# Kernel tuning notes

Hardware: AMD Instinct MI355X
Metric: run time of the kernel (lower is better)

## Reference

```python
import jax, jax.numpy as jnp
import numpy as np

B, N, F, H, E = 32, 512, 256, 1024, 8192
LN_EPS = 1e-5


def setup_inputs() -> dict:
    key = jax.random.key(0)
    ks = jax.random.split(key, 8)
    s = 0.02
    return {
        "node_features": jax.random.normal(ks[0], (B, N, F), jnp.float32),
        "edge_indexd": jax.random.randint(ks[1], (2, E), 0, N, jnp.int64),
        "edge_weights": jax.random.uniform(ks[2], (B, E), jnp.float32),
        "ln_gamma": jnp.ones((F,), jnp.float32),
        "ln_beta": jnp.zeros((F,), jnp.float32),
        "w1": jax.random.normal(ks[3], (H, N), jnp.float32) * s,
        "b1": jnp.zeros((H,), jnp.float32),
        "w2": jax.random.normal(ks[4], (N, H), jnp.float32) * s,
        "b2": jnp.zeros((N,), jnp.float32),
    }


def _laplacian(edge_idx, w):
    # w: [E] edge weights for one graph; edge_idx: [2, E]
    w = jnp.clip(w, 0.0, 1.0)
    # sparse_coo_tensor(...).to_dense() sums duplicate indices -> scatter-add
    A = jnp.zeros((N, N), w.dtype).at[edge_idx[0], edge_idx[1]].add(w)
    A = (A + A.T) * 0.5
    deg = jnp.clip(A.sum(axis=1), 1e-6, None)
    dis = deg ** -0.5  # finite since deg >= 1e-6
    L = jnp.eye(N, dtype=w.dtype) - dis[:, None] * A * dis[None, :]
    L = (L + L.T) * 0.5 + 1e-6 * jnp.eye(N, dtype=w.dtype)
    return L


def _forward(node_features, edge_indexd, edge_weights, ln_gamma, ln_beta, w1, b1, w2, b2):
    L = jax.vmap(lambda w: _laplacian(edge_indexd, w))(edge_weights)  # [B,N,N]
    # eigh is applied to L.detach() in the original -> stop_gradient
    eigvals, eigvecs = jnp.linalg.eigh(jax.lax.stop_gradient(L))  # [B,N], [B,N,N]

    # LayerNorm over feat_dim
    mu = node_features.mean(-1, keepdims=True)
    var = node_features.var(-1, keepdims=True)
    x = (node_features - mu) * jax.lax.rsqrt(var + LN_EPS) * ln_gamma + ln_beta
    x_residual = x
    x = jax.nn.relu(x)

    # x1 = eigvecs^T @ x : [B,N,F]
    x1 = jnp.einsum('bnk,bnf->bkf', eigvecs, x)
    # MLP on eigenvalues (dropout inactive in eval)
    h = jax.nn.relu(eigvals @ w1.T + b1)  # [B,H]
    ev_feat = h @ w2.T + b2               # [B,N]
    x1 = x1 * ev_feat[:, :, None]
    out = jnp.einsum('bnk,bkf->bnf', eigvecs, x1) + x_residual
    return out


def reference(node_features, edge_indexd, edge_weights, ln_gamma, ln_beta, w1, b1, w2, b2):
    return _forward(node_features, edge_indexd, edge_weights, ln_gamma, ln_beta, w1, b1, w2, b2)
```

## Files before the change

kernel.cpp:

```cpp
#include <hip/hip_runtime.h>
#include <math.h>

#define BDIM 32
#define NDIM 512
#define FDIM 256
#define HDIM 1024
#define EDIM 8192
#define PCH  8192
#define CLTH 1.2e-4f
#define NB   16
#define BCOLS 16

__device__ __forceinline__ float waveRedSum(float v){
#pragma unroll
  for(int o=32;o>0;o>>=1) v += __shfl_down(v,o,64);
  return v;
}

__device__ __forceinline__ float rnd_f(int g, int i){
  unsigned s = (unsigned)g*1315423911u ^ (unsigned)i*2654435761u;
  s ^= s>>13; s *= 2246822519u; s ^= s>>16;
  return (float)(s & 0xFFFF)*(1.f/65536.f) - 0.5f;
}

__global__ __launch_bounds__(1024) void k_detect(const unsigned* __restrict__ e, int* __restrict__ flag){
  int t = threadIdx.x;
  float c = 0.f;
  for(int i=t;i<EDIM;i+=1024) if(e[2*i+1] != 0u) c += 1.f;
  c = waveRedSum(c);
  __shared__ float r[16];
  if((t&63)==0) r[t>>6]=c;
  __syncthreads();
  if(t==0){ float s=0; for(int z=0;z<16;z++) s+=r[z]; flag[0] = (s>64.f)?1:0; }
}

__global__ __launch_bounds__(256) void k_scatter(const float* __restrict__ ew, const int* __restrict__ eidx,
                                                 const int* __restrict__ flag, float* __restrict__ A){
  int t = blockIdx.x*256 + threadIdx.x;
  int b = t>>13, e = t&(EDIM-1);
  int i, j;
  if(flag[0]){ i = eidx[e]; j = eidx[EDIM+e]; }
  else       { i = eidx[2*e]; j = eidx[2*(EDIM+e)]; }
  i &= 511; j &= 511;
  float w = ew[(size_t)b*EDIM + e];
  w = 0.5f*fminf(fmaxf(w,0.f),1.f);
  float* Ab = A + (size_t)b*NDIM*NDIM;
  atomicAdd(Ab + (size_t)i*NDIM + j, w);
  atomicAdd(Ab + (size_t)j*NDIM + i, w);
}

__global__ __launch_bounds__(256) void k_degree(const float* __restrict__ A, float* __restrict__ dis){
  int wid = threadIdx.x>>6, lane = threadIdx.x&63;
  int row = blockIdx.x*4 + wid;
  const float* Ar = A + (size_t)row*NDIM;
  float s = 0.f;
  for(int j=lane;j<NDIM;j+=64) s += Ar[j];
  s = waveRedSum(s);
  if(lane==0) dis[row] = rsqrtf(fmaxf(s, 1e-6f));
}

__global__ __launch_bounds__(256) void k_lap(float* __restrict__ A, const float* __restrict__ dis){
  size_t t = (size_t)blockIdx.x*256 + threadIdx.x;
  size_t nn = (size_t)NDIM*NDIM;
  int b = (int)(t / nn); size_t rem = t % nn;
  int i = (int)(rem / NDIM), j = (int)(rem % NDIM);
  float v = -dis[b*NDIM+i]*dis[b*NDIM+j]*A[t];
  if(i==j) v += 1.f + 1e-6f;
  A[t] = v;
}

__global__ __launch_bounds__(256) void k_ln(const float* __restrict__ nf, const float* __restrict__ g,
                                            const float* __restrict__ be, float* __restrict__ X){
  int wid = threadIdx.x>>6, lane = threadIdx.x&63;
  int row = blockIdx.x*4 + wid;
  const float4* r4 = (const float4*)(nf + (size_t)row*FDIM);
  float4 v = r4[lane];
  float s  = v.x+v.y+v.z+v.w;
  float s2 = v.x*v.x+v.y*v.y+v.z*v.z+v.w*v.w;
  s = waveRedSum(s); s2 = waveRedSum(s2);
  s = __shfl(s,0,64); s2 = __shfl(s2,0,64);
  float mean = s*(1.f/FDIM);
  float var  = s2*(1.f/FDIM) - mean*mean;
  float inv  = rsqrtf(var + 1e-5f);
  float4 gg = ((const float4*)g)[lane];
  float4 bb = ((const float4*)be)[lane];
  float4 o;
  o.x = (v.x-mean)*inv*gg.x + bb.x;
  o.y = (v.y-mean)*inv*gg.y + bb.y;
  o.z = (v.z-mean)*inv*gg.z + bb.z;
  o.w = (v.w-mean)*inv*gg.w + bb.w;
  ((float4*)(X + (size_t)row*FDIM))[lane] = o;
}

__global__ __launch_bounds__(512,1) void k_tridiag(float* __restrict__ A, float* __restrict__ U,
                                                   float* __restrict__ dia, float* __restrict__ off,
                                                   float* __restrict__ tau){
  const int b = blockIdx.x, t = threadIdx.x;
  float* Ab = A + (size_t)b*NDIM*NDIM;
  float* Ub = U + (size_t)b*NDIM*NDIM;
  __shared__ __align__(16) float Up[NB][NDIM];
  __shared__ __align__(16) float Wp[NB][NDIM];
  __shared__ __align__(16) float ps[4][NDIM];
  __shared__ float dW[NB], dU[NB];
  __shared__ float sig_s, pd_s, x0_s;
  const int lane = t&63;
  const int cc = t&127, rg = t>>7;
  if(t==0){ sig_s = 0.f; pd_s = 0.f; }

  for(int k0=0; k0<NDIM-2; k0+=NB){
    const int ne = (NB < NDIM-2-k0)? NB : (NDIM-2-k0);
    for(int q=0;q<NB;q++){ Up[q][t]=0.f; Wp[q][t]=0.f; }
    __syncthreads();
    for(int p=0;p<ne;p++){
      const int k = k0+p;
      float v = 0.f;
      if(t>k){
        v = Ab[(size_t)k*NDIM + t];
        for(int q=0;q<p;q++) v -= Up[q][k]*Wp[q][t] + Wp[q][k]*Up[q][t];
      }
      if(t<NB){ dW[t]=0.f; dU[t]=0.f; }
      if(t==0) pd_s = 0.f;
      if(t==k+1) x0_s = v;
      float ssq = (t>=k+2)? v*v : 0.f;
      ssq = waveRedSum(ssq);
      if(lane==0) atomicAdd(&sig_s, ssq);
      __syncthreads();
      const float sigma = sig_s, x0 = x0_s;
      float tk = 0.f, inv = 0.f, beta = x0;
      if(sigma > 1e-26f){
        beta = -copysignf(sqrtf(x0*x0+sigma), x0);
        tk = (beta-x0)/beta; inv = 1.f/(x0-beta);
      }
      const float u_t = (t>=k+2)? v*inv : ((t==k+1 && sigma>1e-26f)? 1.f : 0.f);
      Up[p][t] = u_t;
      for(int q=0;q<p;q++){
        float pw = waveRedSum(Wp[q][t]*u_t);
        float pu = waveRedSum(Up[q][t]*u_t);
        if(lane==0){ atomicAdd(&dW[q],pw); atomicAdd(&dU[q],pu); }
      }
      __syncthreads();
      if(t==0) sig_s = 0.f;
      {
        float4 acc = {0.f,0.f,0.f,0.f};
        const int j0 = 4*cc;
        if(j0+3 > k){
          const float* basep = Ab + j0;
          const int ib0 = (k+1)&~31;
          const int i1 = rg*4, i2 = 16+rg*4;
          const float* ap = basep + (size_t)ib0*NDIM;
          float4 c0 = *(const float4*)(ap + (size_t)(i1  )*NDIM);
          float4 c1 = *(const float4*)(ap + (size_t)(i1+1)*NDIM);
          float4 c2 = *(const float4*)(ap + (size_t)(i1+2)*NDIM);
          float4 c3 = *(const float4*)(ap + (size_t)(i1+3)*NDIM);
          float4 d0 = *(const float4*)(ap + (size_t)(i2  )*NDIM);
          float4 d1 = *(const float4*)(ap + (size_t)(i2+1)*NDIM);
          float4 d2 = *(const float4*)(ap + (size_t)(i2+2)*NDIM);
          float4 d3 = *(const float4*)(ap + (size_t)(i2+3)*NDIM);
          for(int ib=ib0; ib<NDIM; ib+=32){
            float4 n0=c0,n1=c1,n2=c2,n3=c3,m0=d0,m1=d1,m2=d2,m3=d3;
            if(ib+32 < NDIM){
              const float* an = basep + (size_t)(ib+32)*NDIM;
              n0 = *(const float4*)(an + (size_t)(i1  )*NDIM);
              n1 = *(const float4*)(an + (size_t)(i1+1)*NDIM);
              n2 = *(const float4*)(an + (size_t)(i1+2)*NDIM);
              n3 = *(const float4*)(an + (size_t)(i1+3)*NDIM);
              m0 = *(const float4*)(an + (size_t)(i2  )*NDIM);
              m1 = *(const float4*)(an + (size_t)(i2+1)*NDIM);
              m2 = *(const float4*)(an + (size_t)(i2+2)*NDIM);
              m3 = *(const float4*)(an + (size_t)(i2+3)*NDIM);
            }
            float4 u1 = *(const float4*)&Up[p][ib+i1];
            float4 u2 = *(const float4*)&Up[p][ib+i2];
            acc.x += c0.x*u1.x + c1.x*u1.y + c2.x*u1.z + c3.x*u1.w
                   + d0.x*u2.x + d1.x*u2.y + d2.x*u2.z + d3.x*u2.w;
            acc.y += c0.y*u1.x + c1.y*u1.y + c2.y*u1.z + c3.y*u1.w
                   + d0.y*u2.x + d1.y*u2.y + d2.y*u2.z + d3.y*u2.w;
            acc.z += c0.z*u1.x + c1.z*u1.y + c2.z*u1.z + c3.z*u1.w
                   + d0.z*u2.x + d1.z*u2.y + d2.z*u2.z + d3.z*u2.w;
            acc.w += c0.w*u1.x + c1.w*u1.y + c2.w*u1.z + c3.w*u1.w
                   + d0.w*u2.x + d1.w*u2.y + d2.w*u2.z + d3.w*u2.w;
            c0=n0; c1=n1; c2=n2; c3=n3; d0=m0; d1=m1; d2=m2; d3=m3;
          }
        }
        *(float4*)&ps[rg][4*cc] = acc;
      }
      __syncthreads();
      float py = ps[0][t]+ps[1][t]+ps[2][t]+ps[3][t];
      float corr = 0.f;
      for(int q=0;q<p;q++) corr += Up[q][t]*dW[q] + Wp[q][t]*dU[q];
      float pv = tk*(py - corr);
      float pdp = waveRedSum(pv*u_t);
      if(lane==0) atomicAdd(&pd_s, pdp);
      __syncthreads();
      float hh = 0.5f*tk*pd_s;
      float w_t = (t>k)? (pv - hh*u_t) : 0.f;
      Wp[p][t] = w_t;
      if(t>k) Ub[(size_t)k*NDIM + (t-k-1)] = u_t;
      if(t==0){
        off[(size_t)b*NDIM+k] = beta; tau[(size_t)b*NDIM+k] = tk;
        float dk = Ab[(size_t)k*NDIM+k];
        for(int q=0;q<p;q++) dk -= 2.f*Up[q][k]*Wp[q][k];
        dia[(size_t)b*NDIM+k]=dk;
      }
      __syncthreads();
    }
    {
      const int r0 = k0+ne;
      const int rbase = r0 & ~15;
      const int cstart = rbase>>2;
      if(cc >= cstart){
        const int j0 = 4*cc;
        for(int rt=rbase; rt<NDIM; rt+=16){
          const int i0 = rt + rg*4;
          float* a0 = Ab + (size_t)i0*NDIM + j0;
          float4 v0 = *(float4*)(a0);
          float4 v1 = *(float4*)(a0+NDIM);
          float4 v2 = *(float4*)(a0+2*NDIM);
          float4 v3 = *(float4*)(a0+3*NDIM);
          #pragma unroll 4
          for(int q=0;q<ne;q++){
            float4 Ui = *(const float4*)&Up[q][i0];
            float4 Wi = *(const float4*)&Wp[q][i0];
            float4 Uj = *(const float4*)&Up[q][j0];
            float4 Wj = *(const float4*)&Wp[q][j0];
            v0.x -= Ui.x*Wj.x + Wi.x*Uj.x; v0.y -= Ui.x*Wj.y + Wi.x*Uj.y; v0.z -= Ui.x*Wj.z + Wi.x*Uj.z; v0.w -= Ui.x*Wj.w + Wi.x*Uj.w;
            v1.x -= Ui.y*Wj.x + Wi.y*Uj.x; v1.y -= Ui.y*Wj.y + Wi.y*Uj.y; v1.z -= Ui.y*Wj.z + Wi.y*Uj.z; v1.w -= Ui.y*Wj.w + Wi.y*Uj.w;
            v2.x -= Ui.z*Wj.x + Wi.z*Uj.x; v2.y -= Ui.z*Wj.y + Wi.z*Uj.y; v2.z -= Ui.z*Wj.z + Wi.z*Uj.z; v2.w -= Ui.z*Wj.w + Wi.z*Uj.w;
            v3.x -= Ui.w*Wj.x + Wi.w*Uj.x; v3.y -= Ui.w*Wj.y + Wi.w*Uj.y; v3.z -= Ui.w*Wj.z + Wi.w*Uj.z; v3.w -= Ui.w*Wj.w + Wi.w*Uj.w;
          }
          *(float4*)(a0)        = v0;
          *(float4*)(a0+NDIM)   = v1;
          *(float4*)(a0+2*NDIM) = v2;
          *(float4*)(a0+3*NDIM) = v3;
        }
      }
    }
    __syncthreads();
  }
  if(t==0){
    dia[(size_t)b*NDIM+NDIM-2] = Ab[(size_t)(NDIM-2)*NDIM+NDIM-2];
    dia[(size_t)b*NDIM+NDIM-1] = Ab[(size_t)(NDIM-1)*NDIM+NDIM-1];
    off[(size_t)b*NDIM+NDIM-2] = Ab[(size_t)(NDIM-2)*NDIM+NDIM-1];
    off[(size_t)b*NDIM+NDIM-1] = 0.f;
    tau[(size_t)b*NDIM+NDIM-2]=0.f; tau[(size_t)b*NDIM+NDIM-1]=0.f;
  }
}

__global__ __launch_bounds__(512) void k_bisect(const float* __restrict__ dia, const float* __restrict__ off,
                                                float* __restrict__ lam){
  int b = blockIdx.x, t = threadIdx.x;
  __shared__ float ds[NDIM], e2[NDIM];
  __shared__ float red[16];
  __shared__ float slo, shi;
  ds[t] = dia[(size_t)b*NDIM+t];
  float ev = (t<NDIM-1)? off[(size_t)b*NDIM+t] : 0.f;
  e2[t] = ev*ev;
  __syncthreads();
  float el = (t>0)? sqrtf(e2[t-1]) : 0.f;
  float er = fabsf(ev);
  float lo = ds[t]-el-er, hi = ds[t]+el+er;
#pragma unroll
  for(int o=32;o>0;o>>=1){ lo = fminf(lo,__shfl_down(lo,o,64)); hi = fmaxf(hi,__shfl_down(hi,o,64)); }
  if((t&63)==0){ red[t>>6]=lo; red[8+(t>>6)]=hi; }
  __syncthreads();
  if(t==0){
    float L=red[0], H=red[8];
    for(int z=1;z<8;z++){ L=fminf(L,red[z]); H=fmaxf(H,red[8+z]); }
    slo = L-1e-3f; shi = H+1e-3f;
  }
  __syncthreads();
  float lo2 = slo, hi2 = shi;
  for(int it=0; it<30; ++it){
    float mid = 0.5f*(lo2+hi2);
    float q = ds[0]-mid; int c = (q<0.f)?1:0;
    for(int i=1;i<NDIM;i++){
      float dn = (fabsf(q)<1e-10f)? ((q<0.f)?-1e-10f:1e-10f) : q;
      q = ds[i]-mid - __fdividef(e2[i-1], dn);
      c += (q<0.f)?1:0;
    }
    if(c<=t) lo2=mid; else hi2=mid;
  }
  lam[(size_t)b*NDIM+t] = 0.5f*(lo2+hi2);
}

__global__ __launch_bounds__(64) void k_stein(const float* __restrict__ dia, const float* __restrict__ off,
                                              const float* __restrict__ lam, float* __restrict__ W,
                                              float* __restrict__ fac, float* __restrict__ xs, int chunk){
  int p = blockIdx.x*64 + threadIdx.x;
  int g = chunk*PCH + p;
  int b = g >> 9, j = g & 511;
  __shared__ float ds[NDIM], es[NDIM];
  for(int i=threadIdx.x;i<NDIM;i+=64){ ds[i]=dia[(size_t)b*NDIM+i]; es[i]=off[(size_t)b*NDIM+i]; }
  __syncthreads();
  float lm = lam[(size_t)b*NDIM+j] + (float)((j%5)-2)*1.2e-7f;
  float* fu = fac + p;
  float* fm = fac + (size_t)PCH*NDIM + p;
  float* f1a = xs + p;
  float ai = ds[0]-lm, bi = es[0];
  for(int ib=0; ib<NDIM-1; ib+=8){
    const int lim = (NDIM-1-ib < 8)? NDIM-1-ib : 8;
    float dsb[8], esb[8], enb[8];
    #pragma unroll
    for(int z=0;z<8;z++){
      int i = ib+z; bool vz = z<lim;
      dsb[z] = vz? ds[i+1] : 0.f;
      esb[z] = vz? es[i]   : 0.f;
      enb[z] = (vz && i<NDIM-2)? es[i+1] : 0.f;
    }
    #pragma unroll
    for(int z=0;z<8;z++){
      if(z<lim){
        int i = ib+z;
        float ci = esb[z], an = dsb[z]-lm, bn = enb[z];
        float uu, mmenc, s1;
        if(fabsf(ai) >= fabsf(ci)){
          float aa = (fabsf(ai)<1e-12f)? ((ai<0.f)?-1e-12f:1e-12f) : ai;
          float mm = __fdividef(ci, aa);
          uu=aa; mmenc=mm; s1=bi;
          ai = an - mm*bi; bi = bn;
        } else {
          float cch = (fabsf(ci)<1e-12f)? ((ci<0.f)?-1e-12f:1e-12f) : ci;
          float mm = __fdividef(ai, cch);
          uu=cch; mmenc=mm+3.f; s1=an;
          ai = bi - mm*an; bi = -mm*bn;
        }
        fu[(size_t)i*PCH]=__fdividef(1.f,uu);
        fm[(size_t)i*PCH]=mmenc;
        f1a[(size_t)i*PCH]=s1;
      }
    }
  }
  { float aa = (fabsf(ai)<1e-12f)? ((ai<0.f)?-1e-12f:1e-12f) : ai; fu[(size_t)(NDIM-1)*PCH]=__fdividef(1.f,aa); }
  float* Wb = W + (size_t)b*NDIM*NDIM + j;
  float scale = 1.f;
  for(int it=0; it<3; ++it){
    float yi = (it==0)? rnd_f(g,0) : Wb[0]*scale;
    for(int ib=0; ib<NDIM-1; ib+=8){
      const int lim = (NDIM-1-ib < 8)? NDIM-1-ib : 8;
      float wn[8], me[8];
      #pragma unroll
      for(int z=0;z<8;z++){
        int i = ib+z; bool vz = z<lim;
        wn[z] = vz? ((it==0)? rnd_f(g,i+1) : Wb[(size_t)(i+1)*NDIM]*scale) : 0.f;
        me[z] = vz? fm[(size_t)i*PCH] : 0.f;
      }
      #pragma unroll
      for(int z=0;z<8;z++){
        if(z<lim){
          int i = ib+z;
          float enc = me[z]; bool sw = enc>1.5f; float mm = sw? enc-3.f : enc;
          float yn = wn[z];
          if(sw){ float tmp=yi; yi=yn; yn=tmp; }
          yn -= mm*yi;
          Wb[(size_t)i*NDIM] = yi;
          yi = yn;
        }
      }
    }
    float nrm, xp1, xp2;
    {
      float xi = yi * fu[(size_t)(NDIM-1)*PCH];
      Wb[(size_t)(NDIM-1)*NDIM]=xi; nrm = xi*xi; xp2=0.f; xp1=xi;
    }
    for(int ib=NDIM-2; ib>=0; ib-=8){
      const int lim = (ib+1 < 8)? ib+1 : 8;
      float yv[8], ru[8], me[8], f1b[8];
      #pragma unroll
      for(int z=0;z<8;z++){
        int i = ib-z; bool vz = z<lim;
        yv[z]  = vz? Wb[(size_t)i*NDIM] : 0.f;
        ru[z]  = vz? fu[(size_t)i*PCH] : 0.f;
        me[z]  = vz? fm[(size_t)i*PCH] : 0.f;
        f1b[z] = vz? f1a[(size_t)i*PCH] : 0.f;
      }
      #pragma unroll
      for(int z=0;z<8;z++){
        if(z<lim){
          int i = ib-z;
          bool sw = me[z]>1.5f;
          float f2 = sw? ((i<NDIM-2)? es[i+1] : 0.f) : 0.f;
          float xi = (yv[z] - f1b[z]*xp1 - f2*xp2)*ru[z];
          Wb[(size_t)i*NDIM]=xi; nrm += xi*xi;
          xp2=xp1; xp1=xi;
        }
      }
    }
    scale = rsqrtf(fmaxf(nrm,1e-30f));
  }
  for(int ib=0; ib<NDIM; ib+=8){
    float vz[8];
    #pragma unroll
    for(int z=0;z<8;z++) vz[z] = Wb[(size_t)(ib+z)*NDIM];
    #pragma unroll
    for(int z=0;z<8;z++) Wb[(size_t)(ib+z)*NDIM] = vz[z]*scale;
  }
}

__global__ __launch_bounds__(512) void k_mgs(const float* __restrict__ lam, float* __restrict__ W){
  int b = blockIdx.x, t = threadIdx.x;
  __shared__ int cstart[NDIM];
  __shared__ unsigned char brk[NDIM];
  __shared__ float red[8];
  __shared__ float sbc;
  const float* lb = lam + (size_t)b*NDIM;
  float* Wb = W + (size_t)b*NDIM*NDIM;
  brk[t] = (t==0)? 1 : ((lb[t]-lb[t-1] > CLTH)? 1 : 0);
  __syncthreads();
  if(t==0){ int s=0; for(int j=0;j<NDIM;j++){ if(brk[j]) s=j; cstart[j]=s; } }
  __syncthreads();
  for(int j=1;j<NDIM;j++){
    int s = cstart[j];
    if(s==j) continue;
    for(int q=s;q<j;q++){
      float pd = 0.f;
      pd = Wb[(size_t)t*NDIM+q]*Wb[(size_t)t*NDIM+j];
      pd = waveRedSum(pd);
      if((t&63)==0) red[t>>6]=pd;
      __syncthreads();
      if(t==0){ float s2=0; for(int z=0;z<8;z++) s2+=red[z]; sbc=s2; }
      __syncthreads();
      float dt = sbc;
      Wb[(size_t)t*NDIM+j] -= dt*Wb[(size_t)t*NDIM+q];
      __syncthreads();
    }
    float v = Wb[(size_t)t*NDIM+j];
    float pn = waveRedSum(v*v);
    if((t&63)==0) red[t>>6]=pn;
    __syncthreads();
    if(t==0){ float s2=0; for(int z=0;z<8;z++) s2+=red[z]; sbc=s2; }
    __syncthreads();
    Wb[(size_t)t*NDIM+j] = v*rsqrtf(fmaxf(sbc,1e-20f));
    __syncthreads();
  }
}

__global__ __launch_bounds__(512,4) void k_backt(float* __restrict__ W, const float* __restrict__ U,
                                                 const float* __restrict__ tau){
  __shared__ float S[NDIM][BCOLS+1];
  __shared__ float Up[NB][516];
  __shared__ float Gp[NB][NB+1];
  __shared__ float Tm[NB][NB+1];
  __shared__ float Yp[2][NB][NB+1];
  __shared__ float Z16[NB][NB+1];
  __shared__ float tls[NB];
  const int t = threadIdx.x;
  int b = blockIdx.x >> 5, slab = blockIdx.x & 31;
  int c0 = slab*BCOLS;
  float* Wb = W + (size_t)b*NDIM*NDIM;
  const float* Ub = U + (size_t)b*NDIM*NDIM;
  for(int l=t; l<NDIM*BCOLS; l+=512){
    int i = l>>4, c = l&15;
    S[i][c] = Wb[(size_t)i*NDIM + c0 + c];
  }
  __syncthreads();
  for(int k0 = ((NDIM-3)/NB)*NB; k0>=0; k0-=NB){
    for(int l=t; l<NB*NDIM; l+=512){
      int q = l>>9, i = l&511;
      int k = k0+q;
      float v = 0.f;
      if(k < NDIM-2 && i > k) v = Ub[(size_t)k*NDIM + (i-k-1)];
      Up[q][i] = v;
    }
    if(t<NB) tls[t] = (k0+t < NDIM-2)? tau[(size_t)b*NDIM + k0 + t] : 0.f;
    if(t<NB*(NB+1)) ((float*)Gp)[t] = 0.f;
    __syncthreads();
    if(t < 480){
      int pp = t>>2, sub = t&3;
      int pj=1, pr=pp;
      while(pr >= pj){ pr -= pj; pj++; }
      int s = pr, jj = pj;
      float acc = 0.f;
      for(int i=k0+1+sub; i<NDIM; i+=4) acc += Up[s][i]*Up[jj][i];
      atomicAdd(&Gp[s][jj], acc);
    }
    __syncthreads();
    if(t < 16){
      int a = t;
      for(int j=0;j<NB;j++){
        float v;
        if(a==j) v = tls[j];
        else if(a<j){
          float s2 = 0.f;
          for(int s=a; s<j; s++) s2 += Tm[a][s]*Gp[s][j];
          v = -tls[j]*s2;
        } else v = 0.f;
        Tm[a][j] = v;
      }
    }
    __syncthreads();
    {
      int q=(t>>4)&15, c=t&15, half=t>>8;
      float a0=0.f, a1=0.f;
      int i = k0+1+half;
      for(; i+2<NDIM; i+=4){ a0 += Up[q][i]*S[i][c]; a1 += Up[q][i+2]*S[i+2][c]; }
      for(; i<NDIM; i+=2) a0 += Up[q][i]*S[i][c];
      Yp[half][q][c] = a0+a1;
    }
    __syncthreads();
    if(t < 256){
      int a=t>>4, c=t&15;
      float acc=0.f;
      #pragma unroll
      for(int j=0;j<NB;j++) acc += Tm[a][j]*(Yp[0][j][c]+Yp[1][j][c]);
      Z16[a][c]=acc;
    }
    __syncthreads();
    {
      int rg=t>>4, c=t&15;
      float zc[NB];
      #pragma unroll
      for(int q=0;q<NB;q++) zc[q]=Z16[q][c];
      for(int i=k0+1+rg; i<NDIM; i+=32){
        float s2=0.f;
        #pragma unroll
        for(int q=0;q<NB;q++) s2 += Up[q][i]*zc[q];
        S[i][c] -= s2;
      }
    }
    __syncthreads();
  }
  for(int l=t; l<NDIM*BCOLS; l+=512){
    int i = l>>4, c = l&15;
    Wb[(size_t)i*NDIM + c0 + c] = S[i][c];
  }
}

__global__ __launch_bounds__(256) void k_mlp1(const float* __restrict__ lam, const float* __restrict__ w1,
                                              const float* __restrict__ b1, float* __restrict__ h){
  int wid = threadIdx.x>>6, lane = threadIdx.x&63;
  int j = blockIdx.x*4 + wid, b = blockIdx.y;
  const float* lb = lam + (size_t)b*NDIM;
  const float* wr = w1 + (size_t)j*NDIM;
  float acc = 0.f;
  for(int k=lane;k<NDIM;k+=64) acc += lb[k]*wr[k];
  acc = waveRedSum(acc);
  if(lane==0) h[(size_t)b*HDIM + j] = fmaxf(acc + b1[j], 0.f);
}
__global__ __launch_bounds__(256) void k_mlp2(const float* __restrict__ h, const float* __restrict__ w2,
                                              const float* __restrict__ b2, float* __restrict__ evb){
  int wid = threadIdx.x>>6, lane = threadIdx.x&63;
  int n = blockIdx.x*4 + wid, b = blockIdx.y;
  const float* hb = h + (size_t)b*HDIM;
  const float* wr = w2 + (size_t)n*HDIM;
  float acc = 0.f;
  for(int k=lane;k<HDIM;k+=64) acc += hb[k]*wr[k];
  acc = waveRedSum(acc);
  if(lane==0) evb[(size_t)b*NDIM + n] = acc + b2[n];
}

__global__ __launch_bounds__(256) void k_gemm1(const float* __restrict__ Z, const float* __restrict__ X,
                                               const float* __restrict__ evb, float* __restrict__ X1){
  int b = blockIdx.z;
  int i0 = blockIdx.y*64, f0 = blockIdx.x*64;
  const float* Zb = Z + (size_t)b*NDIM*NDIM;
  const float* Xb = X + (size_t)b*NDIM*FDIM;
  __shared__ float As[32][65], Bs[32][65];
  int tx = threadIdx.x & 15, ty = threadIdx.x >> 4;
  float acc[4][4] = {};
  for(int n0=0;n0<NDIM;n0+=32){
    for(int l=threadIdx.x; l<32*64; l+=256){
      int dn = l>>6, dc = l&63;
      As[dn][dc] = Zb[(size_t)(n0+dn)*NDIM + i0+dc];
      Bs[dn][dc] = fmaxf(Xb[(size_t)(n0+dn)*FDIM + f0+dc], 0.f);
    }
    __syncthreads();
#pragma unroll
    for(int dn=0;dn<32;dn++){
      float a[4], bb[4];
#pragma unroll
      for(int z=0;z<4;z++){ a[z]=As[dn][ty*4+z]; bb[z]=Bs[dn][tx*4+z]; }
#pragma unroll
      for(int p=0;p<4;p++)
#pragma unroll
        for(int q=0;q<4;q++) acc[p][q] += a[p]*bb[q];
    }
    __syncthreads();
  }
#pragma unroll
  for(int p=0;p<4;p++){
    int i = i0 + ty*4 + p;
    float s = evb[(size_t)b*NDIM + i];
    float4 o = { acc[p][0]*s, acc[p][1]*s, acc[p][2]*s, acc[p][3]*s };
    *(float4*)(X1 + ((size_t)b*NDIM + i)*FDIM + f0 + tx*4) = o;
  }
}

__global__ __launch_bounds__(256) void k_gemm2(const float* __restrict__ Z, const float* __restrict__ X1,
                                               const float* __restrict__ X, float* __restrict__ outp){
  int b = blockIdx.z;
  int n0 = blockIdx.y*64, f0 = blockIdx.x*64;
  const float* Zb = Z + (size_t)b*NDIM*NDIM;
  const float* X1b = X1 + (size_t)b*NDIM*FDIM;
  __shared__ float As[32][65], Bs[32][65];
  int tx = threadIdx.x & 15, ty = threadIdx.x >> 4;
  float acc[4][4] = {};
  for(int i0=0;i0<NDIM;i0+=32){
    for(int l=threadIdx.x; l<32*64; l+=256){
      int di = l&31, dn = l>>5;
      As[di][dn] = Zb[(size_t)(n0+dn)*NDIM + i0+di];
    }
    for(int l=threadIdx.x; l<32*64; l+=256){
      int di = l>>6, df = l&63;
      Bs[di][df] = X1b[(size_t)(i0+di)*FDIM + f0+df];
    }
    __syncthreads();
#pragma unroll
    for(int dk=0;dk<32;dk++){
      float a[4], bb[4];
#pragma unroll
      for(int z=0;z<4;z++){ a[z]=As[dk][ty*4+z]; bb[z]=Bs[dk][tx*4+z]; }
#pragma unroll
      for(int p=0;p<4;p++)
#pragma unroll
        for(int q=0;q<4;q++) acc[p][q] += a[p]*bb[q];
    }
    __syncthreads();
  }
#pragma unroll
  for(int p=0;p<4;p++){
    size_t ro = ((size_t)b*NDIM + n0+ty*4+p)*FDIM + f0 + tx*4;
    float4 xr = *(const float4*)(X + ro);
    float4 o = { acc[p][0]+xr.x, acc[p][1]+xr.y, acc[p][2]+xr.z, acc[p][3]+xr.w };
    *(float4*)(outp + ro) = o;
  }
}

extern "C" void kernel_launch(void* const* d_in, const int* in_sizes, int n_in,
                              void* d_out, int out_size, void* d_ws, size_t ws_size,
                              hipStream_t stream) {
  (void)in_sizes; (void)n_in; (void)out_size; (void)ws_size;
  const float* nf  = (const float*)d_in[0];
  const int*   eidx= (const int*)d_in[1];
  const float* ew  = (const float*)d_in[2];
  const float* lng = (const float*)d_in[3];
  const float* lnb = (const float*)d_in[4];
  const float* w1  = (const float*)d_in[5];
  const float* b1  = (const float*)d_in[6];
  const float* w2  = (const float*)d_in[7];
  const float* b2  = (const float*)d_in[8];

  float* ws = (float*)d_ws;
  const size_t NN = (size_t)NDIM*NDIM;
  float* A   = ws;
  float* U   = A  + (size_t)BDIM*NN;
  float* W   = U  + (size_t)BDIM*NN;
  float* X   = W  + (size_t)BDIM*NN;
  float* X1  = X  + (size_t)BDIM*NDIM*FDIM;
  float* dia = X1 + (size_t)BDIM*NDIM*FDIM;
  float* off = dia + (size_t)BDIM*NDIM;
  float* tau = off + (size_t)BDIM*NDIM;
  float* lam = tau + (size_t)BDIM*NDIM;
  float* dis = lam + (size_t)BDIM*NDIM;
  float* hbf = dis + (size_t)BDIM*NDIM;
  float* evb = hbf + (size_t)BDIM*HDIM;
  int*   flag= (int*)(evb + (size_t)BDIM*NDIM);

  hipMemsetAsync(A, 0, (size_t)BDIM*NN*sizeof(float), stream);
  k_detect <<<1, 1024, 0, stream>>>((const unsigned*)eidx, flag);
  k_scatter<<<(BDIM*EDIM)/256, 256, 0, stream>>>(ew, eidx, flag, A);
  k_degree <<<(BDIM*NDIM)/4, 256, 0, stream>>>(A, dis);
  k_lap    <<<(unsigned)((size_t)BDIM*NN/256), 256, 0, stream>>>(A, dis);
  k_ln     <<<(BDIM*NDIM)/4, 256, 0, stream>>>(nf, lng, lnb, X);
  k_tridiag<<<BDIM, 512, 0, stream>>>(A, U, dia, off, tau);
  k_bisect <<<BDIM, 512, 0, stream>>>(dia, off, lam);
  k_mlp1   <<<dim3(HDIM/4, BDIM), 256, 0, stream>>>(lam, w1, b1, hbf);
  k_mlp2   <<<dim3(NDIM/4, BDIM), 256, 0, stream>>>(hbf, w2, b2, evb);
  for(int c=0;c<(BDIM*NDIM)/PCH;c++)
    k_stein<<<PCH/64, 64, 0, stream>>>(dia, off, lam, W, A , X1 , c);
  k_mgs    <<<BDIM, 512, 0, stream>>>(lam, W);
  k_backt  <<<BDIM*32, 512, 0, stream>>>(W, U, tau);
  k_gemm1  <<<dim3(FDIM/64, NDIM/64, BDIM), 256, 0, stream>>>(W, X, evb, X1);
  k_gemm2  <<<dim3(FDIM/64, NDIM/64, BDIM), 256, 0, stream>>>(W, X1, X, (float*)d_out);
}
```

Measured before the change: 9.986 ms.

## Defer Householder w correction and cut barriers in blocked tridiagonalization

```diff
diff --git a/kernel.cpp b/kernel.cpp
--- a/kernel.cpp
+++ b/kernel.cpp
@@ -101,31 +101,35 @@
   __shared__ __align__(16) float Up[NB][NDIM];
   __shared__ __align__(16) float Wp[NB][NDIM];
   __shared__ __align__(16) float ps[4][NDIM];
-  __shared__ float dW[NB], dU[NB];
+  __shared__ float dW[NB], dU[NB], hh_s[NB], dg_s[NB];
   __shared__ float sig_s, pd_s, x0_s;
-  const int lane = t&63;
+  const int lane = t&63, wid = t>>6;
   const int cc = t&127, rg = t>>7;
   if(t==0){ sig_s = 0.f; pd_s = 0.f; }
+  __syncthreads();
+  float hprev = 0.f, rnext = 0.f;
 
   for(int k0=0; k0<NDIM-2; k0+=NB){
     const int ne = (NB < NDIM-2-k0)? NB : (NDIM-2-k0);
-    for(int q=0;q<NB;q++){ Up[q][t]=0.f; Wp[q][t]=0.f; }
-    __syncthreads();
+    if(t<ne) dg_s[t] = Ab[(size_t)(k0+t)*NDIM + (k0+t)];
     for(int p=0;p<ne;p++){
       const int k = k0+p;
       float v = 0.f;
       if(t>k){
-        v = Ab[(size_t)k*NDIM + t];
-        for(int q=0;q<p;q++) v -= Up[q][k]*Wp[q][t] + Wp[q][k]*Up[q][t];
-      }
-      if(t<NB){ dW[t]=0.f; dU[t]=0.f; }
-      if(t==0) pd_s = 0.f;
+        v = (p==0)? Ab[(size_t)k*NDIM + t] : rnext;
+        for(int q=0;q<p;q++){
+          float hq = (q==p-1)? hprev : hh_s[q];
+          float uqk = Up[q][k], wqk = Wp[q][k];
+          v -= uqk*Wp[q][t] + (wqk - 2.f*hq*uqk)*Up[q][t];
+        }
+      }
       if(t==k+1) x0_s = v;
       float ssq = (t>=k+2)? v*v : 0.f;
       ssq = waveRedSum(ssq);
       if(lane==0) atomicAdd(&sig_s, ssq);
       __syncthreads();
       const float sigma = sig_s, x0 = x0_s;
+      if(t==0) pd_s = 0.f;
       float tk = 0.f, inv = 0.f, beta = x0;
       if(sigma > 1e-26f){
         beta = -copysignf(sqrtf(x0*x0+sigma), x0);
@@ -133,13 +137,22 @@
       }
       const float u_t = (t>=k+2)? v*inv : ((t==k+1 && sigma>1e-26f)? 1.f : 0.f);
       Up[p][t] = u_t;
-      for(int q=0;q<p;q++){
-        float pw = waveRedSum(Wp[q][t]*u_t);
-        float pu = waveRedSum(Up[q][t]*u_t);
-        if(lane==0){ atomicAdd(&dW[q],pw); atomicAdd(&dU[q],pu); }
-      }
       __syncthreads();
       if(t==0) sig_s = 0.f;
+      if(p+1<ne) rnext = Ab[(size_t)(k+1)*NDIM + t];
+      for(int q=wid; q<p; q+=8){
+        float du=0.f, dwr=0.f;
+        for(int l=lane; l<NDIM; l+=64){
+          float up_ = Up[p][l];
+          du  += Up[q][l]*up_;
+          dwr += Wp[q][l]*up_;
+        }
+        du = waveRedSum(du); dwr = waveRedSum(dwr);
+        if(lane==0){
+          float hq = (q==p-1)? hprev : hh_s[q];
+          dU[q] = du; dW[q] = dwr - hq*du;
+        }
+      }
       {
         float4 acc = {0.f,0.f,0.f,0.f};
         const int j0 = 4*cc;
@@ -187,23 +200,36 @@
       __syncthreads();
       float py = ps[0][t]+ps[1][t]+ps[2][t]+ps[3][t];
       float corr = 0.f;
-      for(int q=0;q<p;q++) corr += Up[q][t]*dW[q] + Wp[q][t]*dU[q];
+      for(int q=0;q<p;q++){
+        float hq = (q==p-1)? hprev : hh_s[q];
+        float duq = dU[q];
+        corr += Up[q][t]*(dW[q] - hq*duq) + Wp[q][t]*duq;
+      }
       float pv = tk*(py - corr);
+      Wp[p][t] = pv;
       float pdp = waveRedSum(pv*u_t);
       if(lane==0) atomicAdd(&pd_s, pdp);
+      if(t>k) Ub[(size_t)k*NDIM + (t-k-1)] = u_t;
+      if(t==0){ off[(size_t)b*NDIM+k] = beta; tau[(size_t)b*NDIM+k] = tk; }
       __syncthreads();
-      float hh = 0.5f*tk*pd_s;
-      float w_t = (t>k)? (pv - hh*u_t) : 0.f;
-      Wp[p][t] = w_t;
-      if(t>k) Ub[(size_t)k*NDIM + (t-k-1)] = u_t;
       if(t==0){
-        off[(size_t)b*NDIM+k] = beta; tau[(size_t)b*NDIM+k] = tk;
-        float dk = Ab[(size_t)k*NDIM+k];
-        for(int q=0;q<p;q++) dk -= 2.f*Up[q][k]*Wp[q][k];
-        dia[(size_t)b*NDIM+k]=dk;
-      }
-      __syncthreads();
-    }
+        float dk = dg_s[p];
+        for(int q=0;q<p;q++){
+          float hq = (q==p-1)? hprev : hh_s[q];
+          float uqk = Up[q][k];
+          dk -= 2.f*uqk*(Wp[q][k] - hq*uqk);
+        }
+        dia[(size_t)b*NDIM+k] = dk;
+      }
+      hprev = 0.5f*tk*pd_s;
+      if(t==0) hh_s[p] = hprev;
+    }
+    __syncthreads();
+    for(int q=0;q<ne;q++){
+      float hq = (q==ne-1)? hprev : hh_s[q];
+      Wp[q][t] -= hq*Up[q][t];
+    }
+    __syncthreads();
     {
       const int r0 = k0+ne;
       const int rbase = r0 & ~15;
```

Result: faster. 8.642 ms, median of 2 (-13.5%).
